# Kernel optimization log

Measured on AMD Instinct MI355X. Metric: run time of the kernel, lower is better.

Reference implementation:

```python
import jax, jax.numpy as jnp
import numpy as np
import math

VOCAB, SEQ, D_MODEL, H, D_FF, N_LAYERS = 32000, 2048, 768, 12, 3072, 6
D_K = D_MODEL // H
EPS = 1e-7


def _pos_encoding(seq, d):
    pos = jnp.arange(seq, dtype=jnp.float32)[:, None]
    i = jnp.arange(d)[None, :]
    rates = 1.0 / jnp.power(10000.0, (2 * (i // 2)).astype(jnp.float32) / d)
    ang = pos * rates
    return jnp.where(i % 2 == 0, jnp.sin(ang), jnp.cos(ang))  # [seq, d]


def _layernorm(x, alpha, beta):
    # faithful to source: scalar alpha/beta, population std, std+eps in denom
    mean = jnp.mean(x, axis=-1, keepdims=True)
    std = jnp.std(x, axis=-1, keepdims=True)
    return alpha * (x - mean) / (std + EPS) + beta


def setup_inputs() -> dict:
    key = jax.random.key(0)
    ks = jax.random.split(key, 16)
    s = 0.02
    d, f, n = D_MODEL, D_FF, N_LAYERS
    inp = {
        'tokens': jax.random.randint(ks[0], (2, SEQ), 0, VOCAB),
        'emb': jax.random.normal(ks[1], (VOCAB, d), jnp.float32) * s,
        'Wq': jax.random.normal(ks[2], (n, d, d), jnp.float32) * s,
        'bq': jnp.zeros((n, d), jnp.float32),
        'Wk': jax.random.normal(ks[3], (n, d, d), jnp.float32) * s,
        'bk': jnp.zeros((n, d), jnp.float32),
        'Wv': jax.random.normal(ks[4], (n, d, d), jnp.float32) * s,
        'bv': jnp.zeros((n, d), jnp.float32),
        'Wo': jax.random.normal(ks[5], (n, d, d), jnp.float32) * s,
        'bo': jnp.zeros((n, d), jnp.float32),
        'W1': jax.random.normal(ks[6], (n, d, f), jnp.float32) * s,
        'b1': jnp.zeros((n, f), jnp.float32),
        'W2': jax.random.normal(ks[7], (n, f, d), jnp.float32) * s,
        'b2': jnp.zeros((n, d), jnp.float32),
        'ln_alpha': jnp.ones((n, 2), jnp.float32),  # source inits alpha AND beta to ones
        'ln_beta': jnp.ones((n, 2), jnp.float32),
    }
    return inp


def reference(tokens, emb, Wq, bq, Wk, bk, Wv, bv, Wo, bo, W1, b1, W2, b2, ln_alpha, ln_beta):
    B, S = tokens.shape
    x = emb[tokens] * math.sqrt(D_MODEL)          # [B,S,D]
    pe = _pos_encoding(SEQ, D_MODEL)[:S]
    x = x + (x + pe)
    for l in range(N_LAYERS):
        # --- self-attention sublayer (pre-norm then residual add) ---
        h = _layernorm(x, ln_alpha[l, 0], ln_beta[l, 0])
        q = (h @ Wq[l] + bq[l]).reshape(B, S, H, D_K)
        k = (h @ Wk[l] + bk[l]).reshape(B, S, H, D_K)
        v = (h @ Wv[l] + bv[l]).reshape(B, S, H, D_K)
        scores = jnp.einsum('bqhd,bkhd->bhqk', q, k) / math.sqrt(D_K)
        attn = jax.nn.softmax(scores, axis=-1)
        o = jnp.einsum('bhqk,bkhd->bqhd', attn, v).reshape(B, S, D_MODEL)
        x = x + (o @ Wo[l] + bo[l])
        # --- feed-forward sublayer ---
        h = _layernorm(x, ln_alpha[l, 1], ln_beta[l, 1])
        ff = jax.nn.relu(h @ W1[l] + b1[l]) @ W2[l] + b2[l]
        x = x + ff
    return x
```

## Files before the change

### kernel.cpp

```cpp
#include <hip/hip_runtime.h>
#include <cstdint>

#define SEQ 2048
#define DM 768
#define NH 12
#define DKH 64
#define DFF 3072
#define NL 6
#define NTOK 4096

typedef __attribute__((ext_vector_type(8))) short bf16x8;
typedef __attribute__((ext_vector_type(4))) float f32x4;

static __device__ __forceinline__ unsigned short f2b(float f) {
    unsigned int u = __builtin_bit_cast(unsigned int, f);
    unsigned int lsb = (u >> 16) & 1;
    u += 0x7fffu + lsb;
    return (unsigned short)(u >> 16);
}

static __device__ __forceinline__ unsigned int cvtpk2(float a, float b) {
    unsigned int r;
    asm("v_cvt_pk_bf16_f32 %0, %1, %2" : "=v"(r) : "v"(a), "v"(b));
    return r;
}

__global__ __launch_bounds__(256) void embed_k(const int* __restrict__ tokens,
                                               const float* __restrict__ emb,
                                               float* __restrict__ x)
{
    int srow = blockIdx.y;
    int d = blockIdx.x * 256 + threadIdx.x;
    int s = srow & (SEQ - 1);
    int tok = tokens[srow];
    float val = 2.0f * 27.712812921102035f * emb[(size_t)tok * DM + d];
    int half2 = (d >> 1) * 2;
    float freq = expf(-(float)half2 * (9.210340371976184f / (float)DM));
    float ang = (float)s * freq;
    val += (d & 1) ? cosf(ang) : sinf(ang);
    x[(size_t)srow * DM + d] = val;
}

__global__ __launch_bounds__(256) void ln_k(const float* __restrict__ x,
                                            unsigned short* __restrict__ h,
                                            const float* __restrict__ alpha_p,
                                            const float* __restrict__ beta_p)
{
    int lane = threadIdx.x & 63;
    int wv = threadIdx.x >> 6;
    int row = blockIdx.x * 4 + wv;
    const float* xr = x + (size_t)row * DM;
    float4 v0 = *(const float4*)&xr[lane * 4];
    float4 v1 = *(const float4*)&xr[256 + lane * 4];
    float4 v2 = *(const float4*)&xr[512 + lane * 4];
    float s  = v0.x + v0.y + v0.z + v0.w + v1.x + v1.y + v1.z + v1.w
             + v2.x + v2.y + v2.z + v2.w;
    float sq = v0.x*v0.x + v0.y*v0.y + v0.z*v0.z + v0.w*v0.w
             + v1.x*v1.x + v1.y*v1.y + v1.z*v1.z + v1.w*v1.w
             + v2.x*v2.x + v2.y*v2.y + v2.z*v2.z + v2.w*v2.w;
#pragma unroll
    for (int m = 1; m < 64; m <<= 1) {
        s  += __shfl_xor(s, m);
        sq += __shfl_xor(sq, m);
    }
    float mean = s * (1.0f / DM);
    float var  = sq * (1.0f / DM) - mean * mean;
    float stdv = sqrtf(fmaxf(var, 0.0f));
    float scale = (*alpha_p) / (stdv + 1e-7f);
    float beta  = *beta_p;
    unsigned short* hr = h + (size_t)row * DM;
    ushort4 o;
    o.x = f2b((v0.x - mean) * scale + beta); o.y = f2b((v0.y - mean) * scale + beta);
    o.z = f2b((v0.z - mean) * scale + beta); o.w = f2b((v0.w - mean) * scale + beta);
    *(ushort4*)&hr[lane * 4] = o;
    o.x = f2b((v1.x - mean) * scale + beta); o.y = f2b((v1.y - mean) * scale + beta);
    o.z = f2b((v1.z - mean) * scale + beta); o.w = f2b((v1.w - mean) * scale + beta);
    *(ushort4*)&hr[256 + lane * 4] = o;
    o.x = f2b((v2.x - mean) * scale + beta); o.y = f2b((v2.y - mean) * scale + beta);
    o.z = f2b((v2.z - mean) * scale + beta); o.w = f2b((v2.w - mean) * scale + beta);
    *(ushort4*)&hr[512 + lane * 4] = o;
}

struct WCAll { const float* src[6]; unsigned short* dst[6]; };
__global__ __launch_bounds__(256) void wconv_all_k(WCAll p)
{
    int t = blockIdx.x;
    const float* W; unsigned short* Wt; int K, N, bn, bk;
    if (t < 2304) {
        int mat = t / 576, rem = t % 576;
        W = p.src[mat]; Wt = p.dst[mat]; K = 768; N = 768;
        bn = (rem % 24) * 32; bk = (rem / 24) * 32;
    } else if (t < 4608) {
        int rem = t - 2304;
        W = p.src[4]; Wt = p.dst[4]; K = 768; N = 3072;
        bn = (rem % 96) * 32; bk = (rem / 96) * 32;
    } else {
        int rem = t - 4608;
        W = p.src[5]; Wt = p.dst[5]; K = 3072; N = 768;
        bn = (rem % 24) * 32; bk = (rem / 24) * 32;
    }
    __shared__ float tt[32][33];
    int tx = threadIdx.x & 31, ty = threadIdx.x >> 5;
#pragma unroll
    for (int i = 0; i < 4; ++i)
        tt[ty * 4 + i][tx] = W[(size_t)(bk + ty * 4 + i) * N + bn + tx];
    __syncthreads();
    int n_l = threadIdx.x >> 3;
    int k_l = (threadIdx.x & 7) * 4;
    ushort4 o;
    o.x = f2b(tt[k_l + 0][n_l]); o.y = f2b(tt[k_l + 1][n_l]);
    o.z = f2b(tt[k_l + 2][n_l]); o.w = f2b(tt[k_l + 3][n_l]);
    *(ushort4*)&Wt[(size_t)(bn + n_l) * K + bk + k_l] = o;
}

template<int OUT_MODE>
__device__ __forceinline__ void gemm_mfma_body(
    const unsigned short* __restrict__ A,
    const unsigned short* __restrict__ Bt,
    const float* __restrict__ bias,
    void* __restrict__ Cv,
    int N, int K, int kbeg, int kend, int bm, int bn)
{
    __shared__ unsigned short As[128][64];
    __shared__ unsigned short Bs[128][64];
    const int tid = threadIdx.x;
    const int lane = tid & 63;
    const int w = tid >> 6;
    const int wm = (w >> 1) << 6;
    const int wn = (w & 1) << 6;
    const int rgrp = lane >> 3;
    const int chunk = (lane & 7) ^ rgrp;
    const size_t a_src = (size_t)(bm + w * 32 + rgrp) * K + chunk * 8;
    const size_t b_src = (size_t)(bn + w * 32 + rgrp) * K + chunk * 8;

    f32x4 acc[4][4] = {};

    for (int kt = kbeg; kt < kend; kt += 64) {
        __syncthreads();
#pragma unroll
        for (int i = 0; i < 4; ++i) {
            __builtin_amdgcn_global_load_lds(
                (const __attribute__((address_space(1))) void*)(A + a_src + (size_t)(i * 8) * K + kt),
                (__attribute__((address_space(3))) void*)&As[w * 32 + i * 8][0], 16, 0, 0);
            __builtin_amdgcn_global_load_lds(
                (const __attribute__((address_space(1))) void*)(Bt + b_src + (size_t)(i * 8) * K + kt),
                (__attribute__((address_space(3))) void*)&Bs[w * 32 + i * 8][0], 16, 0, 0);
        }
        __syncthreads();
#pragma unroll
        for (int kk = 0; kk < 2; ++kk) {
            bf16x8 af[4], bfr[4];
            const int kb = kk * 64 + ((lane >> 4) << 4);
#pragma unroll
            for (int i = 0; i < 4; ++i) {
                int m = wm + i * 16 + (lane & 15);
                af[i] = *(const bf16x8*)((const char*)&As[0][0] + m * 128 + (kb ^ ((m & 7) << 4)));
                int n = wn + i * 16 + (lane & 15);
                bfr[i] = *(const bf16x8*)((const char*)&Bs[0][0] + n * 128 + (kb ^ ((n & 7) << 4)));
            }
            __builtin_amdgcn_s_setprio(1);
#pragma unroll
            for (int i = 0; i < 4; ++i)
#pragma unroll
                for (int j = 0; j < 4; ++j)
                    acc[i][j] = __builtin_amdgcn_mfma_f32_16x16x32_bf16(af[i], bfr[j], acc[i][j], 0, 0, 0);
            __builtin_amdgcn_s_setprio(0);
        }
    }
    const int cl = lane & 15, rg = lane >> 4;
#pragma unroll
    for (int i = 0; i < 4; ++i) {
        int row0 = bm + wm + i * 16 + rg * 4;
#pragma unroll
        for (int j = 0; j < 4; ++j) {
            int col = bn + wn + j * 16 + cl;
            float bv = (OUT_MODE == 5 && kbeg > 0) ? 0.0f : bias[col];
            if (OUT_MODE == 4) {
                int bb = row0 >> 11;
                int s  = row0 & 2047;
                int hh = col >> 6, d = col & 63;
                ushort4 o;
                o.x = f2b(acc[i][j][0] + bv); o.y = f2b(acc[i][j][1] + bv);
                o.z = f2b(acc[i][j][2] + bv); o.w = f2b(acc[i][j][3] + bv);
                *(ushort4*)&((unsigned short*)Cv)[(((size_t)(bb * 12 + hh) * 64 + d) << 11) + s] = o;
            } else {
#pragma unroll
                for (int r = 0; r < 4; ++r) {
                    float val = acc[i][j][r] + bv;
                    size_t idx = (size_t)(row0 + r) * N + col;
                    if (OUT_MODE == 2) {
                        ((unsigned short*)Cv)[idx] = f2b(fmaxf(val, 0.0f));
                    } else if (OUT_MODE == 3) {
                        ((unsigned short*)Cv)[idx] = f2b(val);
                    } else if (OUT_MODE == 5) {
                        atomicAdd(&((float*)Cv)[idx], val);
                    } else {
                        ((float*)Cv)[idx] += val;
                    }
                }
            }
        }
    }
}

template<int OUT_MODE>
__global__ __launch_bounds__(256) void gemm_b(const unsigned short* __restrict__ A,
                                              const unsigned short* __restrict__ Bt,
                                              const float* __restrict__ bias,
                                              void* __restrict__ C, int N, int K)
{
    gemm_mfma_body<OUT_MODE>(A, Bt, bias, C, N, K, 0, K, blockIdx.y * 128, blockIdx.x * 128);
}

__global__ __launch_bounds__(256) void gemm_sk(const unsigned short* __restrict__ A,
                                               const unsigned short* __restrict__ Bt,
                                               const float* __restrict__ bias,
                                               float* __restrict__ C, int N, int K)
{
    int half = K >> 1;
    gemm_mfma_body<5>(A, Bt, bias, C, N, K, blockIdx.z * half, blockIdx.z * half + half,
                      blockIdx.y * 128, blockIdx.x * 128);
}

struct QKVArgsB {
    const unsigned short *wq, *wk, *wv;
    const float *bq, *bk, *bv;
    unsigned short *q, *k, *vt;
};
__global__ __launch_bounds__(256) void gemm_qkv_b(const unsigned short* __restrict__ h, QKVArgsB p)
{
    if (blockIdx.z == 0)
        gemm_mfma_body<3>(h, p.wq, p.bq, p.q, DM, DM, 0, DM, blockIdx.y * 128, blockIdx.x * 128);
    else if (blockIdx.z == 1)
        gemm_mfma_body<3>(h, p.wk, p.bk, p.k, DM, DM, 0, DM, blockIdx.y * 128, blockIdx.x * 128);
    else
        gemm_mfma_body<4>(h, p.wv, p.bv, p.vt, DM, DM, 0, DM, blockIdx.y * 128, blockIdx.x * 128);
}

#define SM_SCALE 0.18033688f
#define DEFER_THR 8.0f
__global__ __launch_bounds__(256) void attn_m(const unsigned short* __restrict__ qg,
                                              const unsigned short* __restrict__ kg,
                                              const unsigned short* __restrict__ vt,
                                              unsigned short* __restrict__ og)
{
    __shared__ unsigned short Ks[2][64 * 64];
    __shared__ unsigned short Vs[2][64 * 64];
    __shared__ unsigned short Ps[4 * 16 * 64];
    const int tid = threadIdx.x;
    const int lane = tid & 63;
    const int w = tid >> 6;
    const int cl = lane & 15, g = lane >> 4;
    const int qt = blockIdx.x, h = blockIdx.y, b = blockIdx.z;
    const int qrow0 = (b << 11) + qt * 64;
    const int krow0 = (b << 11);
    const int srow8 = lane >> 3;
    const int c8 = (lane & 7) ^ srow8;
    const int swz = (cl & 7) << 4;

    bf16x8 qf[2];
#pragma unroll
    for (int sl = 0; sl < 2; ++sl)
        qf[sl] = *(const bf16x8*)(qg + (size_t)(qrow0 + w * 16 + cl) * DM
                                  + h * 64 + sl * 32 + g * 8);

    f32x4 oa[4] = {};
    float m_r = -3.0e38f, l_r = 0.f;

    const unsigned short* ksrc = kg + (size_t)(krow0 + w * 16 + srow8) * DM + h * 64 + c8 * 8;
    const unsigned short* vsrc = vt + ((size_t)((b * 12 + h) * 64) + w * 16 + srow8) * SEQ + c8 * 8;
    char* pbase = (char*)Ps + w * 2048;

#define STAGE(kt_, c_)                                                                         \
    {                                                                                          \
        _Pragma("unroll")                                                                      \
        for (int t = 0; t < 2; ++t) {                                                          \
            __builtin_amdgcn_global_load_lds(                                                  \
                (const __attribute__((address_space(1))) void*)(ksrc + (size_t)((kt_) * 64 + t * 8) * DM), \
                (__attribute__((address_space(3))) void*)&Ks[c_][(w * 16 + t * 8) * 64], 16, 0, 0);        \
            __builtin_amdgcn_global_load_lds(                                                  \
                (const __attribute__((address_space(1))) void*)(vsrc + (size_t)(t * 8) * SEQ + (kt_) * 64), \
                (__attribute__((address_space(3))) void*)&Vs[c_][(w * 16 + t * 8) * 64], 16, 0, 0);        \
        }                                                                                      \
    }

    STAGE(0, 0);
    __syncthreads();

    for (int kt = 0; kt < SEQ / 64; ++kt) {
        const int c = kt & 1;
        if (kt + 1 < SEQ / 64)
            STAGE(kt + 1, c ^ 1);

        f32x4 st[4] = {};
#pragma unroll
        for (int sl = 0; sl < 2; ++sl) {
            bf16x8 kf[4];
#pragma unroll
            for (int ni = 0; ni < 4; ++ni) {
                int row = ni * 16 + cl;
                kf[ni] = *(const bf16x8*)((const char*)&Ks[c][0] + row * 128
                                          + ((sl * 64 + g * 16) ^ ((row & 7) << 4)));
            }
            __builtin_amdgcn_s_setprio(1);
#pragma unroll
            for (int ni = 0; ni < 4; ++ni)
                st[ni] = __builtin_amdgcn_mfma_f32_16x16x32_bf16(kf[ni], qf[sl], st[ni], 0, 0, 0);
            __builtin_amdgcn_s_setprio(0);
        }

        float pmax = -3.0e38f;
#pragma unroll
        for (int ni = 0; ni < 4; ++ni)
#pragma unroll
            for (int r = 0; r < 4; ++r)
                pmax = fmaxf(pmax, st[ni][r]);
        pmax = fmaxf(pmax, __shfl_xor(pmax, 16));
        pmax = fmaxf(pmax, __shfl_xor(pmax, 32));
        pmax *= SM_SCALE;

        if (!__all(pmax <= m_r + DEFER_THR)) {
            float mnew = fmaxf(m_r, pmax);
            float sc = exp2f(m_r - mnew);
            l_r *= sc;
            m_r = mnew;
            float scr[4];
#pragma unroll
            for (int r = 0; r < 4; ++r)
                scr[r] = __shfl(sc, g * 4 + r);
#pragma unroll
            for (int nj = 0; nj < 4; ++nj)
#pragma unroll
                for (int r = 0; r < 4; ++r)
                    oa[nj][r] *= scr[r];
        }

        float rs = 0.f;
        float p[4][4];
#pragma unroll
        for (int ni = 0; ni < 4; ++ni)
#pragma unroll
            for (int r = 0; r < 4; ++r) {
                p[ni][r] = exp2f(fmaf(st[ni][r], SM_SCALE, -m_r));
                rs += p[ni][r];
            }
        rs += __shfl_xor(rs, 16);
        rs += __shfl_xor(rs, 32);
        l_r += rs;

#pragma unroll
        for (int ni = 0; ni < 4; ++ni) {
            uint2 o2;
            o2.x = cvtpk2(p[ni][0], p[ni][1]);
            o2.y = cvtpk2(p[ni][2], p[ni][3]);
            *(uint2*)(pbase + cl * 128 + ((ni * 32 + g * 8) ^ swz)) = o2;
        }
        asm volatile("" ::: "memory");

#pragma unroll
        for (int ks = 0; ks < 2; ++ks) {
            bf16x8 pa, vb[4];
            pa = *(const bf16x8*)(pbase + cl * 128 + ((ks * 64 + g * 16) ^ swz));
#pragma unroll
            for (int nj = 0; nj < 4; ++nj) {
                int row = nj * 16 + cl;
                vb[nj] = *(const bf16x8*)((const char*)&Vs[c][0] + row * 128
                                          + ((ks * 64 + g * 16) ^ ((row & 7) << 4)));
            }
            __builtin_amdgcn_s_setprio(1);
#pragma unroll
            for (int nj = 0; nj < 4; ++nj)
                oa[nj] = __builtin_amdgcn_mfma_f32_16x16x32_bf16(pa, vb[nj], oa[nj], 0, 0, 0);
            __builtin_amdgcn_s_setprio(0);
        }

        __syncthreads();
    }
#undef STAGE

    float linv[4];
#pragma unroll
    for (int r = 0; r < 4; ++r)
        linv[r] = 1.0f / __shfl(l_r, g * 4 + r);
#pragma unroll
    for (int r = 0; r < 4; ++r) {
        int row = qrow0 + w * 16 + g * 4 + r;
#pragma unroll
        for (int nj = 0; nj < 4; ++nj)
            og[(size_t)row * DM + h * 64 + nj * 16 + cl] = f2b(oa[nj][r] * linv[r]);
    }
}

extern "C" void kernel_launch(void* const* d_in, const int* in_sizes, int n_in,
                              void* d_out, int out_size, void* d_ws, size_t ws_size,
                              hipStream_t stream)
{
    const int*   tokens = (const int*)d_in[0];
    const float* emb    = (const float*)d_in[1];
    const float* Wq     = (const float*)d_in[2];
    const float* bq     = (const float*)d_in[3];
    const float* Wk     = (const float*)d_in[4];
    const float* bk     = (const float*)d_in[5];
    const float* Wv     = (const float*)d_in[6];
    const float* bv     = (const float*)d_in[7];
    const float* Wo     = (const float*)d_in[8];
    const float* bo     = (const float*)d_in[9];
    const float* W1     = (const float*)d_in[10];
    const float* b1     = (const float*)d_in[11];
    const float* W2     = (const float*)d_in[12];
    const float* b2     = (const float*)d_in[13];
    const float* ln_a   = (const float*)d_in[14];
    const float* ln_b   = (const float*)d_in[15];

    float* x = (float*)d_out;
    unsigned short* wq_b = (unsigned short*)d_ws;
    unsigned short* wk_b = wq_b + 589824;
    unsigned short* wv_b = wk_b + 589824;
    unsigned short* wo_b = wv_b + 589824;
    unsigned short* w1_b = wo_b + 589824;
    unsigned short* w2_b = w1_b + 2359296;
    unsigned short* h_b  = w2_b + 2359296;
    unsigned short* ob_b = h_b + 3145728;
    unsigned short* ff_b = ob_b + 3145728;
    unsigned short* q_bf = ff_b + 12582912;
    unsigned short* k_bf = q_bf + 3145728;
    unsigned short* vt_b = k_bf + 3145728;

    embed_k<<<dim3(DM / 256, NTOK), 256, 0, stream>>>(tokens, emb, x);

    for (int l = 0; l < NL; ++l) {
        const size_t wsq = (size_t)l * DM * DM;
        const size_t wsf = (size_t)l * DM * DFF;

        WCAll wc;
        wc.src[0] = Wq + wsq; wc.src[1] = Wk + wsq; wc.src[2] = Wv + wsq;
        wc.src[3] = Wo + wsq; wc.src[4] = W1 + wsf; wc.src[5] = W2 + wsf;
        wc.dst[0] = wq_b; wc.dst[1] = wk_b; wc.dst[2] = wv_b;
        wc.dst[3] = wo_b; wc.dst[4] = w1_b; wc.dst[5] = w2_b;
        wconv_all_k<<<6912, 256, 0, stream>>>(wc);

        ln_k<<<NTOK / 4, 256, 0, stream>>>(x, h_b, ln_a + l * 2 + 0, ln_b + l * 2 + 0);

        QKVArgsB p { wq_b, wk_b, wv_b, bq + l * DM, bk + l * DM, bv + l * DM,
                     q_bf, k_bf, vt_b };
        gemm_qkv_b<<<dim3(DM / 128, NTOK / 128, 3), 256, 0, stream>>>(h_b, p);

        attn_m<<<dim3(SEQ / 64, NH, 2), 256, 0, stream>>>(q_bf, k_bf, vt_b, ob_b);

        gemm_sk<<<dim3(DM / 128, NTOK / 128, 2), 256, 0, stream>>>(
            ob_b, wo_b, bo + l * DM, x, DM, DM);

        ln_k<<<NTOK / 4, 256, 0, stream>>>(x, h_b, ln_a + l * 2 + 1, ln_b + l * 2 + 1);

        gemm_b<2><<<dim3(DFF / 128, NTOK / 128), 256, 0, stream>>>(
            h_b, w1_b, b1 + l * DFF, ff_b, DFF, DM);

        gemm_sk<<<dim3(DM / 128, NTOK / 128, 2), 256, 0, stream>>>(
            ff_b, w2_b, b2 + l * DM, x, DM, DFF);
    }
}
```

Measured before the change: 1.323 ms.

## Process 32 query rows per wave in attention to reuse K/V tiles

The attention kernel now gives each wave two 16-row query sub-tiles (128 query rows per block), so every K and V fragment read from LDS feeds twice as many MFMAs. The cross-lane row-sum reduction is moved out of the key loop and done once at the end, and the max shuffle is skipped unless a rescale is needed. In exchange the grid is halved to 384 blocks, which can leave CUs idle or unevenly loaded, and register and LDS use per block goes up.

```diff
diff --git a/kernel.cpp b/kernel.cpp
--- a/kernel.cpp
+++ b/kernel.cpp
@@ -246,30 +246,33 @@
 {
     __shared__ unsigned short Ks[2][64 * 64];
     __shared__ unsigned short Vs[2][64 * 64];
-    __shared__ unsigned short Ps[4 * 16 * 64];
+    __shared__ unsigned short Ps[4 * 32 * 64];
     const int tid = threadIdx.x;
     const int lane = tid & 63;
     const int w = tid >> 6;
     const int cl = lane & 15, g = lane >> 4;
     const int qt = blockIdx.x, h = blockIdx.y, b = blockIdx.z;
-    const int qrow0 = (b << 11) + qt * 64;
+    const int qrow0 = (b << 11) + qt * 128;
     const int krow0 = (b << 11);
     const int srow8 = lane >> 3;
     const int c8 = (lane & 7) ^ srow8;
     const int swz = (cl & 7) << 4;
 
-    bf16x8 qf[2];
-#pragma unroll
-    for (int sl = 0; sl < 2; ++sl)
-        qf[sl] = *(const bf16x8*)(qg + (size_t)(qrow0 + w * 16 + cl) * DM
-                                  + h * 64 + sl * 32 + g * 8);
-
-    f32x4 oa[4] = {};
-    float m_r = -3.0e38f, l_r = 0.f;
+    bf16x8 qf[2][2];
+#pragma unroll
+    for (int mi = 0; mi < 2; ++mi)
+#pragma unroll
+        for (int sl = 0; sl < 2; ++sl)
+            qf[mi][sl] = *(const bf16x8*)(qg + (size_t)(qrow0 + w * 32 + mi * 16 + cl) * DM
+                                          + h * 64 + sl * 32 + g * 8);
+
+    f32x4 oa[2][4] = {};
+    float m_r[2] = { -3.0e38f, -3.0e38f };
+    float l_r[2] = { 0.f, 0.f };
 
     const unsigned short* ksrc = kg + (size_t)(krow0 + w * 16 + srow8) * DM + h * 64 + c8 * 8;
     const unsigned short* vsrc = vt + ((size_t)((b * 12 + h) * 64) + w * 16 + srow8) * SEQ + c8 * 8;
-    char* pbase = (char*)Ps + w * 2048;
+    char* pbase = (char*)Ps + w * 4096;
 
 #define STAGE(kt_, c_)                                                                         \
     {                                                                                          \
@@ -292,7 +295,7 @@
         if (kt + 1 < SEQ / 64)
             STAGE(kt + 1, c ^ 1);
 
-        f32x4 st[4] = {};
+        f32x4 st[2][4] = {};
 #pragma unroll
         for (int sl = 0; sl < 2; ++sl) {
             bf16x8 kf[4];
@@ -304,63 +307,69 @@
             }
             __builtin_amdgcn_s_setprio(1);
 #pragma unroll
+            for (int mi = 0; mi < 2; ++mi)
+#pragma unroll
+                for (int ni = 0; ni < 4; ++ni)
+                    st[mi][ni] = __builtin_amdgcn_mfma_f32_16x16x32_bf16(kf[ni], qf[mi][sl], st[mi][ni], 0, 0, 0);
+            __builtin_amdgcn_s_setprio(0);
+        }
+
+#pragma unroll
+        for (int mi = 0; mi < 2; ++mi) {
+            float pmax = st[mi][0][0];
+#pragma unroll
             for (int ni = 0; ni < 4; ++ni)
-                st[ni] = __builtin_amdgcn_mfma_f32_16x16x32_bf16(kf[ni], qf[sl], st[ni], 0, 0, 0);
-            __builtin_amdgcn_s_setprio(0);
-        }
-
-        float pmax = -3.0e38f;
-#pragma unroll
-        for (int ni = 0; ni < 4; ++ni)
-#pragma unroll
-            for (int r = 0; r < 4; ++r)
-                pmax = fmaxf(pmax, st[ni][r]);
-        pmax = fmaxf(pmax, __shfl_xor(pmax, 16));
-        pmax = fmaxf(pmax, __shfl_xor(pmax, 32));
-        pmax *= SM_SCALE;
-
-        if (!__all(pmax <= m_r + DEFER_THR)) {
-            float mnew = fmaxf(m_r, pmax);
-            float sc = exp2f(m_r - mnew);
-            l_r *= sc;
-            m_r = mnew;
-            float scr[4];
-#pragma unroll
-            for (int r = 0; r < 4; ++r)
-                scr[r] = __shfl(sc, g * 4 + r);
-#pragma unroll
-            for (int nj = 0; nj < 4; ++nj)
 #pragma unroll
                 for (int r = 0; r < 4; ++r)
-                    oa[nj][r] *= scr[r];
-        }
-
-        float rs = 0.f;
-        float p[4][4];
-#pragma unroll
-        for (int ni = 0; ni < 4; ++ni)
-#pragma unroll
-            for (int r = 0; r < 4; ++r) {
-                p[ni][r] = exp2f(fmaf(st[ni][r], SM_SCALE, -m_r));
-                rs += p[ni][r];
-            }
-        rs += __shfl_xor(rs, 16);
-        rs += __shfl_xor(rs, 32);
-        l_r += rs;
-
-#pragma unroll
-        for (int ni = 0; ni < 4; ++ni) {
-            uint2 o2;
-            o2.x = cvtpk2(p[ni][0], p[ni][1]);
-            o2.y = cvtpk2(p[ni][2], p[ni][3]);
-            *(uint2*)(pbase + cl * 128 + ((ni * 32 + g * 8) ^ swz)) = o2;
+                    pmax = fmaxf(pmax, st[mi][ni][r]);
+
+            if (!__all(pmax * SM_SCALE <= m_r[mi] + DEFER_THR)) {
+                float mx = fmaxf(pmax, __shfl_xor(pmax, 16));
+                mx = fmaxf(mx, __shfl_xor(mx, 32));
+                mx *= SM_SCALE;
+                float mnew = fmaxf(m_r[mi], mx);
+                float sc = exp2f(m_r[mi] - mnew);
+                l_r[mi] *= sc;
+                m_r[mi] = mnew;
+                float scr[4];
+#pragma unroll
+                for (int r = 0; r < 4; ++r)
+                    scr[r] = __shfl(sc, g * 4 + r);
+#pragma unroll
+                for (int nj = 0; nj < 4; ++nj)
+#pragma unroll
+                    for (int r = 0; r < 4; ++r)
+                        oa[mi][nj][r] *= scr[r];
+            }
+
+            float rs = 0.f;
+            float p[4][4];
+#pragma unroll
+            for (int ni = 0; ni < 4; ++ni)
+#pragma unroll
+                for (int r = 0; r < 4; ++r) {
+                    p[ni][r] = exp2f(fmaf(st[mi][ni][r], SM_SCALE, -m_r[mi]));
+                    rs += p[ni][r];
+                }
+            l_r[mi] += rs;
+
+            const int prow = mi * 16 + cl;
+#pragma unroll
+            for (int ni = 0; ni < 4; ++ni) {
+                uint2 o2;
+                o2.x = cvtpk2(p[ni][0], p[ni][1]);
+                o2.y = cvtpk2(p[ni][2], p[ni][3]);
+                *(uint2*)(pbase + prow * 128 + ((ni * 32 + g * 8) ^ swz)) = o2;
+            }
         }
         asm volatile("" ::: "memory");
 
 #pragma unroll
         for (int ks = 0; ks < 2; ++ks) {
-            bf16x8 pa, vb[4];
-            pa = *(const bf16x8*)(pbase + cl * 128 + ((ks * 64 + g * 16) ^ swz));
+            bf16x8 pa[2], vb[4];
+#pragma unroll
+            for (int mi = 0; mi < 2; ++mi)
+                pa[mi] = *(const bf16x8*)(pbase + (mi * 16 + cl) * 128 + ((ks * 64 + g * 16) ^ swz));
 #pragma unroll
             for (int nj = 0; nj < 4; ++nj) {
                 int row = nj * 16 + cl;
@@ -369,25 +378,33 @@
             }
             __builtin_amdgcn_s_setprio(1);
 #pragma unroll
+            for (int mi = 0; mi < 2; ++mi)
+#pragma unroll
+                for (int nj = 0; nj < 4; ++nj)
+                    oa[mi][nj] = __builtin_amdgcn_mfma_f32_16x16x32_bf16(pa[mi], vb[nj], oa[mi][nj], 0, 0, 0);
+            __builtin_amdgcn_s_setprio(0);
+        }
+
+        __syncthreads();
+    }
+#undef STAGE
+
+#pragma unroll
+    for (int mi = 0; mi < 2; ++mi) {
+        float ls = l_r[mi];
+        ls += __shfl_xor(ls, 16);
+        ls += __shfl_xor(ls, 32);
+        float linv[4];
+#pragma unroll
+        for (int r = 0; r < 4; ++r)
+            linv[r] = 1.0f / __shfl(ls, g * 4 + r);
+#pragma unroll
+        for (int r = 0; r < 4; ++r) {
+            int row = qrow0 + w * 32 + mi * 16 + g * 4 + r;
+#pragma unroll
             for (int nj = 0; nj < 4; ++nj)
-                oa[nj] = __builtin_amdgcn_mfma_f32_16x16x32_bf16(pa, vb[nj], oa[nj], 0, 0, 0);
-            __builtin_amdgcn_s_setprio(0);
-        }
-
-        __syncthreads();
-    }
-#undef STAGE
-
-    float linv[4];
-#pragma unroll
-    for (int r = 0; r < 4; ++r)
-        linv[r] = 1.0f / __shfl(l_r, g * 4 + r);
-#pragma unroll
-    for (int r = 0; r < 4; ++r) {
-        int row = qrow0 + w * 16 + g * 4 + r;
-#pragma unroll
-        for (int nj = 0; nj < 4; ++nj)
-            og[(size_t)row * DM + h * 64 + nj * 16 + cl] = f2b(oa[nj][r] * linv[r]);
+                og[(size_t)row * DM + h * 64 + nj * 16 + cl] = f2b(oa[mi][nj][r] * linv[r]);
+        }
     }
 }
 
@@ -445,7 +462,7 @@
                      q_bf, k_bf, vt_b };
         gemm_qkv_b<<<dim3(DM / 128, NTOK / 128, 3), 256, 0, stream>>>(h_b, p);
 
-        attn_m<<<dim3(SEQ / 64, NH, 2), 256, 0, stream>>>(q_bf, k_bf, vt_b, ob_b);
+        attn_m<<<dim3(SEQ / 128, NH, 2), 256, 0, stream>>>(q_bf, k_bf, vt_b, ob_b);
 
         gemm_sk<<<dim3(DM / 128, NTOK / 128, 2), 256, 0, stream>>>(
             ob_b, wo_b, bo + l * DM, x, DM, DM);
```

Result: slower. 1.379 ms (+4.2%).

## Compute softmax row sums via MFMA with ones, defer max reduction, swizzle GEMM blocks across XCDs

Applied to the files above, without the earlier changes.

Attention now gets the softmax denominator from an extra MFMA that multiplies the bf16 P tile by a vector of ones, which removes the per-tile scalar sum and its shuffles. The cross-lane max reduction only runs when the deferred-rescale threshold check fails. The GEMM kernels also remap block indices so that neighbouring tiles land on the same XCD for better L2 reuse. In exchange, the denominator is now summed from the bf16-rounded P values, which slightly changes numerics, and each key tile costs extra MFMA work.

```diff
diff --git a/kernel.cpp b/kernel.cpp
--- a/kernel.cpp
+++ b/kernel.cpp
@@ -203,13 +203,23 @@
     }
 }
 
+static __device__ __forceinline__ void xcd_swz(int gx, int& bm, int& bn)
+{
+    int flat = blockIdx.y * gx + blockIdx.x;
+    int nwg = gx * gridDim.y;
+    int wg = (flat & 7) * (nwg >> 3) + (flat >> 3);
+    bm = (wg / gx) * 128;
+    bn = (wg % gx) * 128;
+}
+
 template<int OUT_MODE>
 __global__ __launch_bounds__(256) void gemm_b(const unsigned short* __restrict__ A,
                                               const unsigned short* __restrict__ Bt,
                                               const float* __restrict__ bias,
                                               void* __restrict__ C, int N, int K)
 {
-    gemm_mfma_body<OUT_MODE>(A, Bt, bias, C, N, K, 0, K, blockIdx.y * 128, blockIdx.x * 128);
+    int bm, bn; xcd_swz(gridDim.x, bm, bn);
+    gemm_mfma_body<OUT_MODE>(A, Bt, bias, C, N, K, 0, K, bm, bn);
 }
 
 __global__ __launch_bounds__(256) void gemm_sk(const unsigned short* __restrict__ A,
@@ -217,9 +227,10 @@
                                                const float* __restrict__ bias,
                                                float* __restrict__ C, int N, int K)
 {
+    int bm, bn; xcd_swz(gridDim.x, bm, bn);
     int half = K >> 1;
     gemm_mfma_body<5>(A, Bt, bias, C, N, K, blockIdx.z * half, blockIdx.z * half + half,
-                      blockIdx.y * 128, blockIdx.x * 128);
+                      bm, bn);
 }
 
 struct QKVArgsB {
@@ -229,12 +240,13 @@
 };
 __global__ __launch_bounds__(256) void gemm_qkv_b(const unsigned short* __restrict__ h, QKVArgsB p)
 {
+    int bm, bn; xcd_swz(gridDim.x, bm, bn);
     if (blockIdx.z == 0)
-        gemm_mfma_body<3>(h, p.wq, p.bq, p.q, DM, DM, 0, DM, blockIdx.y * 128, blockIdx.x * 128);
+        gemm_mfma_body<3>(h, p.wq, p.bq, p.q, DM, DM, 0, DM, bm, bn);
     else if (blockIdx.z == 1)
-        gemm_mfma_body<3>(h, p.wk, p.bk, p.k, DM, DM, 0, DM, blockIdx.y * 128, blockIdx.x * 128);
+        gemm_mfma_body<3>(h, p.wk, p.bk, p.k, DM, DM, 0, DM, bm, bn);
     else
-        gemm_mfma_body<4>(h, p.wv, p.bv, p.vt, DM, DM, 0, DM, blockIdx.y * 128, blockIdx.x * 128);
+        gemm_mfma_body<4>(h, p.wv, p.bv, p.vt, DM, DM, 0, DM, bm, bn);
 }
 
 #define SM_SCALE 0.18033688f
@@ -264,8 +276,13 @@
         qf[sl] = *(const bf16x8*)(qg + (size_t)(qrow0 + w * 16 + cl) * DM
                                   + h * 64 + sl * 32 + g * 8);
 
+    bf16x8 ones;
+#pragma unroll
+    for (int j = 0; j < 8; ++j) ones[j] = (short)0x3F80;
+
     f32x4 oa[4] = {};
-    float m_r = -3.0e38f, l_r = 0.f;
+    f32x4 la = {};
+    float m_r = -3.0e38f;
 
     const unsigned short* ksrc = kg + (size_t)(krow0 + w * 16 + srow8) * DM + h * 64 + c8 * 8;
     const unsigned short* vsrc = vt + ((size_t)((b * 12 + h) * 64) + w * 16 + srow8) * SEQ + c8 * 8;
@@ -309,50 +326,42 @@
             __builtin_amdgcn_s_setprio(0);
         }
 
-        float pmax = -3.0e38f;
+        float pmax = st[0][0];
 #pragma unroll
         for (int ni = 0; ni < 4; ++ni)
 #pragma unroll
             for (int r = 0; r < 4; ++r)
                 pmax = fmaxf(pmax, st[ni][r]);
-        pmax = fmaxf(pmax, __shfl_xor(pmax, 16));
-        pmax = fmaxf(pmax, __shfl_xor(pmax, 32));
-        pmax *= SM_SCALE;
-
-        if (!__all(pmax <= m_r + DEFER_THR)) {
-            float mnew = fmaxf(m_r, pmax);
+
+        if (!__all(pmax * SM_SCALE <= m_r + DEFER_THR)) {
+            float mx = fmaxf(pmax, __shfl_xor(pmax, 16));
+            mx = fmaxf(mx, __shfl_xor(mx, 32));
+            mx *= SM_SCALE;
+            float mnew = fmaxf(m_r, mx);
             float sc = exp2f(m_r - mnew);
-            l_r *= sc;
             m_r = mnew;
             float scr[4];
 #pragma unroll
             for (int r = 0; r < 4; ++r)
                 scr[r] = __shfl(sc, g * 4 + r);
 #pragma unroll
-            for (int nj = 0; nj < 4; ++nj)
-#pragma unroll
-                for (int r = 0; r < 4; ++r)
+            for (int r = 0; r < 4; ++r) {
+                la[r] *= scr[r];
+#pragma unroll
+                for (int nj = 0; nj < 4; ++nj)
                     oa[nj][r] *= scr[r];
-        }
-
-        float rs = 0.f;
-        float p[4][4];
-#pragma unroll
-        for (int ni = 0; ni < 4; ++ni)
-#pragma unroll
-            for (int r = 0; r < 4; ++r) {
-                p[ni][r] = exp2f(fmaf(st[ni][r], SM_SCALE, -m_r));
-                rs += p[ni][r];
             }
-        rs += __shfl_xor(rs, 16);
-        rs += __shfl_xor(rs, 32);
-        l_r += rs;
+        }
 
 #pragma unroll
         for (int ni = 0; ni < 4; ++ni) {
+            float p0 = exp2f(fmaf(st[ni][0], SM_SCALE, -m_r));
+            float p1 = exp2f(fmaf(st[ni][1], SM_SCALE, -m_r));
+            float p2 = exp2f(fmaf(st[ni][2], SM_SCALE, -m_r));
+            float p3 = exp2f(fmaf(st[ni][3], SM_SCALE, -m_r));
             uint2 o2;
-            o2.x = cvtpk2(p[ni][0], p[ni][1]);
-            o2.y = cvtpk2(p[ni][2], p[ni][3]);
+            o2.x = cvtpk2(p0, p1);
+            o2.y = cvtpk2(p2, p3);
             *(uint2*)(pbase + cl * 128 + ((ni * 32 + g * 8) ^ swz)) = o2;
         }
         asm volatile("" ::: "memory");
@@ -371,6 +380,7 @@
 #pragma unroll
             for (int nj = 0; nj < 4; ++nj)
                 oa[nj] = __builtin_amdgcn_mfma_f32_16x16x32_bf16(pa, vb[nj], oa[nj], 0, 0, 0);
+            la = __builtin_amdgcn_mfma_f32_16x16x32_bf16(pa, ones, la, 0, 0, 0);
             __builtin_amdgcn_s_setprio(0);
         }
 
@@ -378,16 +388,13 @@
     }
 #undef STAGE
 
-    float linv[4];
-#pragma unroll
-    for (int r = 0; r < 4; ++r)
-        linv[r] = 1.0f / __shfl(l_r, g * 4 + r);
 #pragma unroll
     for (int r = 0; r < 4; ++r) {
+        float linv = 1.0f / la[r];
         int row = qrow0 + w * 16 + g * 4 + r;
 #pragma unroll
         for (int nj = 0; nj < 4; ++nj)
-            og[(size_t)row * DM + h * 64 + nj * 16 + cl] = f2b(oa[nj][r] * linv[r]);
+            og[(size_t)row * DM + h * 64 + nj * 16 + cl] = f2b(oa[nj][r] * linv);
     }
 }
 
```

Result: faster. 1.251 ms (-5.4%).
